# Optimization experiments

Measured on AMD Instinct MI355X. Metric: run time of the kernel, lower is better.

The kernel has to match this reference:

```python
import jax, jax.numpy as jnp
import numpy as np

NODE_FEATURES = 256
HIDDEN = 32
N_NODES = 100000
N_EDGES = 3200000


def _glorot(key, shape):
    fan_in, fan_out = shape[-2], shape[-1]
    lim = (6.0 / (fan_in + fan_out)) ** 0.5
    return jax.random.uniform(key, shape, jnp.float32, -lim, lim)


def setup_inputs() -> dict:
    key = jax.random.key(0)
    ks = jax.random.split(key, 12)
    in_cat = NODE_FEATURES + HIDDEN  # DConv input is cat([X, H])
    x = jax.random.normal(ks[0], (N_NODES, NODE_FEATURES), jnp.float32)
    edge_index = jax.random.randint(ks[1], (2, N_EDGES), 0, N_NODES, jnp.int64)
    return {
        "x": x,
        "edge_index": edge_index,
        # DConv weights have shape (2, K=1, in, out); squeeze K -> (2, in, out)
        "w_z": _glorot(ks[2], (2, in_cat, HIDDEN)),
        "b_z": jnp.zeros((HIDDEN,), jnp.float32),
        "w_r": _glorot(ks[3], (2, in_cat, HIDDEN)),
        "b_r": jnp.zeros((HIDDEN,), jnp.float32),
        "w_h": _glorot(ks[4], (2, in_cat, HIDDEN)),
        "b_h": jnp.zeros((HIDDEN,), jnp.float32),
        # fc head, stored as [in, out]
        "fc1_w": _glorot(ks[5], (HIDDEN, HIDDEN)),
        "fc1_b": jnp.zeros((HIDDEN,), jnp.float32),
        "fc2_w": _glorot(ks[6], (HIDDEN, 1)),
        "fc2_b": jnp.zeros((1,), jnp.float32),
    }


def _dconv_k1(inp, w, b):
    # K=1 DConv: only the k=0 Chebyshev term for both diffusion directions,
    # i.e. no propagation over edges. H = X @ W_out + X @ W_in + bias.
    return inp @ (w[0] + w[1]) + b


def reference(x, edge_index, w_z, b_z, w_r, b_r, w_h, b_h, fc1_w, fc1_b, fc2_w, fc2_b):
    n = x.shape[0]
    h0 = jnp.zeros((n, HIDDEN), x.dtype)  # DCRNN called with H=None -> zeros
    xh0 = jnp.concatenate([x, h0], axis=1)  # [N, F+H]
    z = jax.nn.sigmoid(_dconv_k1(xh0, w_z, b_z))  # update gate
    r = jax.nn.sigmoid(_dconv_k1(xh0, w_r, b_r))  # reset gate
    xrh = jnp.concatenate([x, r * h0], axis=1)
    h_tilde = jnp.tanh(_dconv_k1(xrh, w_h, b_h))
    h = z * h0 + (1.0 - z) * h_tilde  # [N, 32]
    # fc head: Linear-ReLU-Dropout(eval=identity)-Linear-Sigmoid
    hidden = jax.nn.relu(h @ fc1_w + fc1_b)
    out = jax.nn.sigmoid(hidden @ fc2_w + fc2_b)  # [N, 1]
    return out
```

## Files before the change

kernel.cpp:

```cpp
#include <hip/hip_runtime.h>
#include <hip/hip_bf16.h>


#define NF    256
#define NOUT  64
#define MB    128
#define BK    32
#define NTHR  256
#define XPAD  132
#define WPAD  68
#define HPAD  34
#define S_FLOATS 6400

__global__ void prep_W(const float* __restrict__ wz,
                       const float* __restrict__ wh,
                       float* __restrict__ Wp)
{
    int idx = blockIdx.x * blockDim.x + threadIdx.x;
    if (idx >= NF * NOUT) return;
    int k = idx >> 6;
    int j = idx & 63;
    int tx = j >> 2, m = j & 3;
    int o = 2 * tx + (m & 1) + ((m >> 1) << 5);
    const int PLANE = 288 * 32;
    float v;
    if (o < 32) v = wz[k * 32 + o]        + wz[PLANE + k * 32 + o];
    else        v = wh[k * 32 + (o - 32)] + wh[PLANE + k * 32 + (o - 32)];
    Wp[idx] = v;
}

__device__ __forceinline__ float fast_sigmoid(float v) {
    return 1.0f / (1.0f + __expf(-v));
}
__device__ __forceinline__ float fast_tanh(float v) {
    return 1.0f - 2.0f / (1.0f + __expf(2.0f * v));
}

__global__ void __launch_bounds__(NTHR, 4)
rgcn_main(const float* __restrict__ x,
          const float* __restrict__ Wp,
          const float* __restrict__ bz,
          const float* __restrict__ bh,
          const float* __restrict__ fc1w,
          const float* __restrict__ fc1b,
          const float* __restrict__ fc2w,
          const float* __restrict__ fc2b,
          float* __restrict__ out,
          int n_nodes)
{
    __shared__ float S[S_FLOATS];
    float* XsT = S;
    float* Ws  = S + BK * XPAD;

    const int tid   = threadIdx.x;
    const int tx    = tid & 15;
    const int ty    = tid >> 4;
    const int node0 = blockIdx.x * MB;

    float acc[32];
#pragma unroll
    for (int i = 0; i < 32; ++i) acc[i] = 0.0f;

    for (int k0 = 0; k0 < NF; k0 += BK) {
        __syncthreads();
#pragma unroll
        for (int i = 0; i < 4; ++i) {
            int q    = tid + i * NTHR;
            int nn   = q >> 3;
            int slot = q & 7;
            float4 v = make_float4(0.f, 0.f, 0.f, 0.f);
            int gn = node0 + nn;
            if (gn < n_nodes)
                v = *(const float4*)(x + (size_t)gn * NF + k0 + slot * 4);
            XsT[(slot * 4 + 0) * XPAD + nn] = v.x;
            XsT[(slot * 4 + 1) * XPAD + nn] = v.y;
            XsT[(slot * 4 + 2) * XPAD + nn] = v.z;
            XsT[(slot * 4 + 3) * XPAD + nn] = v.w;
        }
#pragma unroll
        for (int i = 0; i < 2; ++i) {
            int q  = tid + i * NTHR;
            int r  = q >> 4;
            int cs = q & 15;
            float4 v = *(const float4*)(Wp + (size_t)(k0 + r) * NOUT + cs * 4);
            *(float4*)(Ws + r * WPAD + cs * 4) = v;
        }
        __syncthreads();

#pragma unroll
        for (int k = 0; k < BK; ++k) {
            const float* xr = XsT + k * XPAD + ty * 8;
            float4 a0 = *(const float4*)(xr);
            float4 a1 = *(const float4*)(xr + 4);
            float4 w  = *(const float4*)(Ws + k * WPAD + tx * 4);
            float a[8] = {a0.x, a0.y, a0.z, a0.w, a1.x, a1.y, a1.z, a1.w};
#pragma unroll
            for (int i = 0; i < 8; ++i) {
                acc[i * 4 + 0] = fmaf(a[i], w.x, acc[i * 4 + 0]);
                acc[i * 4 + 1] = fmaf(a[i], w.y, acc[i * 4 + 1]);
                acc[i * 4 + 2] = fmaf(a[i], w.z, acc[i * 4 + 2]);
                acc[i * 4 + 3] = fmaf(a[i], w.w, acc[i * 4 + 3]);
            }
        }
    }

    __syncthreads();
    float* Hs = S;
    float* Ps = S + MB * HPAD;

    const float bz0 = bz[2 * tx], bz1 = bz[2 * tx + 1];
    const float bh0 = bh[2 * tx], bh1 = bh[2 * tx + 1];
#pragma unroll
    for (int i = 0; i < 8; ++i) {
        int nl = ty * 8 + i;
        float z0 = fast_sigmoid(acc[i * 4 + 0] + bz0);
        float z1 = fast_sigmoid(acc[i * 4 + 1] + bz1);
        float t0 = fast_tanh   (acc[i * 4 + 2] + bh0);
        float t1 = fast_tanh   (acc[i * 4 + 3] + bh1);
        Hs[nl * HPAD + 2 * tx]     = (1.0f - z0) * t0;
        Hs[nl * HPAD + 2 * tx + 1] = (1.0f - z1) * t1;
    }
    __syncthreads();

    const int nl   = tid & (MB - 1);
    const int half = tid >> 7;
    float h[32];
#pragma unroll
    for (int m = 0; m < 8; ++m) {
        float4 v = *(const float4*)(Hs + nl * HPAD + m * 4);
        h[m * 4 + 0] = v.x; h[m * 4 + 1] = v.y;
        h[m * 4 + 2] = v.z; h[m * 4 + 3] = v.w;
    }
    float part = 0.0f;
    for (int jj = 0; jj < 16; ++jj) {
        int j = half * 16 + jj;
        float s = fc1b[j];
#pragma unroll
        for (int o = 0; o < 32; ++o)
            s = fmaf(h[o], fc1w[o * 32 + j], s);
        part = fmaf(fmaxf(s, 0.0f), fc2w[j], part);
    }
    if (half == 1) Ps[nl] = part;
    __syncthreads();
    if (half == 0) {
        int gn = node0 + nl;
        if (gn < n_nodes)
            out[gn] = fast_sigmoid(part + Ps[nl] + fc2b[0]);
    }
}

extern "C" void kernel_launch(void* const* d_in, const int* in_sizes, int n_in,
                              void* d_out, int out_size, void* d_ws, size_t ws_size,
                              hipStream_t stream) {
    const float* x    = (const float*)d_in[0];
    const float* wz   = (const float*)d_in[2];
    const float* bz   = (const float*)d_in[3];
    const float* wh   = (const float*)d_in[6];
    const float* bh   = (const float*)d_in[7];
    const float* fc1w = (const float*)d_in[8];
    const float* fc1b = (const float*)d_in[9];
    const float* fc2w = (const float*)d_in[10];
    const float* fc2b = (const float*)d_in[11];
    float* out = (float*)d_out;
    float* Wp  = (float*)d_ws;

    const int n = in_sizes[0] / NF;

    prep_W<<<(NF * NOUT + 255) / 256, 256, 0, stream>>>(wz, wh, Wp);
    rgcn_main<<<(n + MB - 1) / MB, NTHR, 0, stream>>>(
        x, Wp, bz, bh, fc1w, fc1b, fc2w, fc2b, out, n);
}
```

Baseline: 220.1 us.

## Replace FP32 FMA GEMM with bf16 MFMA 32x32x16 and pre-packed weight fragments

The scalar FP32 outer-product GEMM is replaced by bf16 MFMA instructions. X tiles are converted to bf16 in shared memory in two 128-wide K chunks, and the weights are pre-packed by prep_W into a lane-ordered bf16 fragment layout read directly from global memory. The aim is to cut ALU time and LDS traffic in the main matmul. The cost is reduced precision on both the inputs and the weights, plus a changed epilogue mapping to match the MFMA accumulator layout.

```diff
diff --git a/kernel.cpp b/kernel.cpp
--- a/kernel.cpp
+++ b/kernel.cpp
@@ -2,33 +2,21 @@
 #include <hip/hip_bf16.h>
 
 
-#define NF    256
-#define NOUT  64
-#define MB    128
-#define BK    32
-#define NTHR  256
-#define XPAD  132
-#define WPAD  68
-#define HPAD  34
-#define S_FLOATS 6400
+#define NF     256
+#define NOUT   64
+#define MB     128
+#define NTHR   256
+#define KCHUNK 128
+#define XSTR   132
+#define HPAD   36
 
-__global__ void prep_W(const float* __restrict__ wz,
-                       const float* __restrict__ wh,
-                       float* __restrict__ Wp)
-{
-    int idx = blockIdx.x * blockDim.x + threadIdx.x;
-    if (idx >= NF * NOUT) return;
-    int k = idx >> 6;
-    int j = idx & 63;
-    int tx = j >> 2, m = j & 3;
-    int o = 2 * tx + (m & 1) + ((m >> 1) << 5);
-    const int PLANE = 288 * 32;
-    float v;
-    if (o < 32) v = wz[k * 32 + o]        + wz[PLANE + k * 32 + o];
-    else        v = wh[k * 32 + (o - 32)] + wh[PLANE + k * 32 + (o - 32)];
-    Wp[idx] = v;
+typedef __attribute__((ext_vector_type(8)))  short  short8;
+typedef __attribute__((ext_vector_type(16))) float  floatx16;
+
+__device__ __forceinline__ unsigned f2bf(float f) {
+    __hip_bfloat16 h = __float2bfloat16(f);
+    return (unsigned)*(unsigned short*)&h;
 }
-
 __device__ __forceinline__ float fast_sigmoid(float v) {
     return 1.0f / (1.0f + __expf(-v));
 }
@@ -36,9 +24,28 @@
     return 1.0f - 2.0f / (1.0f + __expf(2.0f * v));
 }
 
+__global__ void prep_W(const float* __restrict__ wz,
+                       const float* __restrict__ wh,
+                       unsigned short* __restrict__ Wf)
+{
+    int idx = blockIdx.x * blockDim.x + threadIdx.x;
+    if (idx >= NF * NOUT) return;
+    int j    = idx & 7;
+    int lane = (idx >> 3) & 63;
+    int nt   = (idx >> 9) & 1;
+    int kt   = idx >> 10;
+    int k = kt * 16 + (lane >> 5) * 8 + j;
+    int o = nt * 32 + (lane & 31);
+    const int PLANE = 288 * 32;
+    float v;
+    if (o < 32) v = wz[k * 32 + o]        + wz[PLANE + k * 32 + o];
+    else        v = wh[k * 32 + (o - 32)] + wh[PLANE + k * 32 + (o - 32)];
+    Wf[idx] = (unsigned short)f2bf(v);
+}
+
 __global__ void __launch_bounds__(NTHR, 4)
 rgcn_main(const float* __restrict__ x,
-          const float* __restrict__ Wp,
+          const unsigned short* __restrict__ Wf,
           const float* __restrict__ bz,
           const float* __restrict__ bh,
           const float* __restrict__ fc1w,
@@ -48,77 +55,65 @@
           float* __restrict__ out,
           int n_nodes)
 {
-    __shared__ float S[S_FLOATS];
-    float* XsT = S;
-    float* Ws  = S + BK * XPAD;
+    __shared__ __align__(16) char S[MB * XSTR * 2];
+    unsigned short* Xb = (unsigned short*)S;
+    float* Hs = (float*)S;
+    float* Ps = (float*)(S + MB * HPAD * 4);
 
     const int tid   = threadIdx.x;
-    const int tx    = tid & 15;
-    const int ty    = tid >> 4;
+    const int lane  = tid & 63;
+    const int wave  = tid >> 6;
+    const int wb    = wave * 32;
     const int node0 = blockIdx.x * MB;
 
-    float acc[32];
-#pragma unroll
-    for (int i = 0; i < 32; ++i) acc[i] = 0.0f;
+    floatx16 acc0 = {};
+    floatx16 acc1 = {};
 
-    for (int k0 = 0; k0 < NF; k0 += BK) {
+    for (int c = 0; c < 2; ++c) {
         __syncthreads();
 #pragma unroll
-        for (int i = 0; i < 4; ++i) {
-            int q    = tid + i * NTHR;
-            int nn   = q >> 3;
-            int slot = q & 7;
+        for (int i = 0; i < 16; ++i) {
+            int nn   = (tid >> 5) + i * 8;
+            int slot = tid & 31;
             float4 v = make_float4(0.f, 0.f, 0.f, 0.f);
             int gn = node0 + nn;
             if (gn < n_nodes)
-                v = *(const float4*)(x + (size_t)gn * NF + k0 + slot * 4);
-            XsT[(slot * 4 + 0) * XPAD + nn] = v.x;
-            XsT[(slot * 4 + 1) * XPAD + nn] = v.y;
-            XsT[(slot * 4 + 2) * XPAD + nn] = v.z;
-            XsT[(slot * 4 + 3) * XPAD + nn] = v.w;
-        }
-#pragma unroll
-        for (int i = 0; i < 2; ++i) {
-            int q  = tid + i * NTHR;
-            int r  = q >> 4;
-            int cs = q & 15;
-            float4 v = *(const float4*)(Wp + (size_t)(k0 + r) * NOUT + cs * 4);
-            *(float4*)(Ws + r * WPAD + cs * 4) = v;
+                v = *(const float4*)(x + (size_t)gn * NF + c * KCHUNK + slot * 4);
+            unsigned lo = f2bf(v.x) | (f2bf(v.y) << 16);
+            unsigned hi = f2bf(v.z) | (f2bf(v.w) << 16);
+            *(uint2*)(Xb + nn * XSTR + slot * 4) = make_uint2(lo, hi);
         }
         __syncthreads();
 
 #pragma unroll
-        for (int k = 0; k < BK; ++k) {
-            const float* xr = XsT + k * XPAD + ty * 8;
-            float4 a0 = *(const float4*)(xr);
-            float4 a1 = *(const float4*)(xr + 4);
-            float4 w  = *(const float4*)(Ws + k * WPAD + tx * 4);
-            float a[8] = {a0.x, a0.y, a0.z, a0.w, a1.x, a1.y, a1.z, a1.w};
-#pragma unroll
-            for (int i = 0; i < 8; ++i) {
-                acc[i * 4 + 0] = fmaf(a[i], w.x, acc[i * 4 + 0]);
-                acc[i * 4 + 1] = fmaf(a[i], w.y, acc[i * 4 + 1]);
-                acc[i * 4 + 2] = fmaf(a[i], w.z, acc[i * 4 + 2]);
-                acc[i * 4 + 3] = fmaf(a[i], w.w, acc[i * 4 + 3]);
-            }
+        for (int kt = 0; kt < 8; ++kt) {
+            int ktg = c * 8 + kt;
+            const uint4* bp = (const uint4*)Wf + (size_t)(ktg * 2) * 64 + lane;
+            uint4 b0u = bp[0];
+            uint4 b1u = bp[64];
+            const unsigned short* ap =
+                Xb + (wb + (lane & 31)) * XSTR + kt * 16 + (lane >> 5) * 8;
+            uint2 alo = *(const uint2*)(ap);
+            uint2 ahi = *(const uint2*)(ap + 4);
+            union { short8 s; uint2 u[2]; } a, b0, b1;
+            a.u[0] = alo; a.u[1] = ahi;
+            b0.u[0] = make_uint2(b0u.x, b0u.y); b0.u[1] = make_uint2(b0u.z, b0u.w);
+            b1.u[0] = make_uint2(b1u.x, b1u.y); b1.u[1] = make_uint2(b1u.z, b1u.w);
+            acc0 = __builtin_amdgcn_mfma_f32_32x32x16_bf16(a.s, b0.s, acc0, 0, 0, 0);
+            acc1 = __builtin_amdgcn_mfma_f32_32x32x16_bf16(a.s, b1.s, acc1, 0, 0, 0);
         }
     }
 
+    const int nc   = lane & 31;
+    const float bzn = bz[nc];
+    const float bhn = bh[nc];
     __syncthreads();
-    float* Hs = S;
-    float* Ps = S + MB * HPAD;
-
-    const float bz0 = bz[2 * tx], bz1 = bz[2 * tx + 1];
-    const float bh0 = bh[2 * tx], bh1 = bh[2 * tx + 1];
 #pragma unroll
-    for (int i = 0; i < 8; ++i) {
-        int nl = ty * 8 + i;
-        float z0 = fast_sigmoid(acc[i * 4 + 0] + bz0);
-        float z1 = fast_sigmoid(acc[i * 4 + 1] + bz1);
-        float t0 = fast_tanh   (acc[i * 4 + 2] + bh0);
-        float t1 = fast_tanh   (acc[i * 4 + 3] + bh1);
-        Hs[nl * HPAD + 2 * tx]     = (1.0f - z0) * t0;
-        Hs[nl * HPAD + 2 * tx + 1] = (1.0f - z1) * t1;
+    for (int r = 0; r < 16; ++r) {
+        int row = (r & 3) + 8 * (r >> 2) + 4 * (lane >> 5);
+        float z = fast_sigmoid(acc0[r] + bzn);
+        float t = fast_tanh   (acc1[r] + bhn);
+        Hs[(wb + row) * HPAD + nc] = (1.0f - z) * t;
     }
     __syncthreads();
 
@@ -162,11 +157,11 @@
     const float* fc2w = (const float*)d_in[10];
     const float* fc2b = (const float*)d_in[11];
     float* out = (float*)d_out;
-    float* Wp  = (float*)d_ws;
+    unsigned short* Wf = (unsigned short*)d_ws;
 
     const int n = in_sizes[0] / NF;
 
-    prep_W<<<(NF * NOUT + 255) / 256, 256, 0, stream>>>(wz, wh, Wp);
+    prep_W<<<(NF * NOUT + 255) / 256, 256, 0, stream>>>(wz, wh, Wf);
     rgcn_main<<<(n + MB - 1) / MB, NTHR, 0, stream>>>(
-        x, Wp, bz, bh, fc1w, fc1b, fc2w, fc2b, out, n);
+        x, Wf, bz, bh, fc1w, fc1b, fc2w, fc2b, out, n);
 }
```

Measured after the change: 206.6 us. 1.07x faster.
